# Performance work log

Measured on AMD Instinct MI355X. Metric: run time of the kernel, lower is better.

Reference implementation:

```python
import jax, jax.numpy as jnp
import numpy as np
from jax import lax

B, S, E = 1, 8192, 64
KSZ = 2
THRESHOLD = 0.0
GAMMA = 1.0
OUT_DIM = 4


def setup_inputs() -> dict:
    key = jax.random.key(0)
    ks = jax.random.split(key, 12)
    def lin(k, fan_in, fan_out):
        bound = 1.0 / np.sqrt(fan_in)
        kw, kb = jax.random.split(k)
        W = jax.random.uniform(kw, (fan_in, fan_out), jnp.float32, -bound, bound)
        b = jax.random.uniform(kb, (fan_out,), jnp.float32, -bound, bound)
        return W, b
    x = jax.random.normal(ks[0], (B, S, E), jnp.float32)
    cb = 1.0 / np.sqrt(KSZ * KSZ)
    conv_w = jax.random.uniform(ks[1], (1, 1, KSZ, KSZ), jnp.float32, -cb, cb)
    conv_b = jax.random.uniform(ks[2], (1,), jnp.float32, -cb, cb)
    Wq, bq = lin(ks[3], E, E)
    Wk, bk = lin(ks[4], E, E)
    Wv, bv = lin(ks[5], E, E)
    Wp, bp = lin(ks[6], E, OUT_DIM)
    return {"x": x, "conv_w": conv_w, "conv_b": conv_b, "Wq": Wq, "bq": bq,
            "Wk": Wk, "bk": bk, "Wv": Wv, "bv": bv, "Wp": Wp, "bp": bp}


def reference(x, conv_w, conv_b, Wq, bq, Wk, bk, Wv, bv, Wp, bp):
    # conv pre-filter: (B,S,E) -> (B,1,E,S) -> scalar per batch
    patched = jnp.transpose(x, (0, 2, 1))[:, None]  # (B,1,E,S)
    logits = lax.conv_general_dilated(
        patched, conv_w, (1, 1), "VALID",
        dimension_numbers=("NCHW", "OIHW", "NCHW")) + conv_b[None, :, None, None]
    conv_feat = jax.nn.sigmoid(logits - THRESHOLD).mean(axis=(2, 3))  # (B,1)
    conv_feat = conv_feat.reshape(B)[:, None]  # (B,1)

    # classical scaled dot-product attention (note: no output projection in source)
    scale = E ** (-0.5)
    q = x @ Wq + bq
    k = x @ Wk + bk
    v = x @ Wv + bv
    scores = jnp.einsum("bse,bte->bst", q, k) * scale  # (B,S,S)
    attn = jax.nn.softmax(scores, axis=-1)
    attn_out = jnp.einsum("bst,bte->bse", attn, v)  # (B,S,E)

    # RBF reweighting (identically 1 since x==y, computed faithfully)
    diff = attn_out - attn_out
    kernel_vals = jnp.exp(-GAMMA * jnp.sum(diff * diff, axis=-1, keepdims=True))  # (B,S,1)

    weighted = attn_out * conv_feat * kernel_vals  # broadcast valid since B==1
    pooled = weighted.mean(axis=1)  # (B,E)
    return pooled @ Wp + bp  # (B,4)
```

## Files before the change

### kernel.cpp

```cpp
#include <hip/hip_runtime.h>
#include <hip/hip_bf16.h>

#define S_LEN 8192
#define E_DIM 64
#define NCONV (63 * 8191)
#define PTS 56
#define SVT (S_LEN + 32)

typedef short short8 __attribute__((ext_vector_type(8)));
typedef float f32x4 __attribute__((ext_vector_type(4)));

__device__ __forceinline__ float ldin(const void* __restrict__ p, int i, int f32flag) {
    return f32flag ? ((const float*)p)[i]
                   : __bfloat162float(((const __hip_bfloat16*)p)[i]);
}
__device__ __forceinline__ float bfbits2f(unsigned int u16bits) {
    union { unsigned int u; float f; } c; c.u = u16bits << 16; return c.f;
}
__device__ __forceinline__ unsigned short f2bfu(float f) {
    __hip_bfloat16 h = __float2bfloat16(f);
    union { __hip_bfloat16 h; unsigned short u; } c; c.h = h; return c.u;
}
__device__ __forceinline__ int hw_bad(unsigned short h) {
    const unsigned int e = (h >> 7) & 0xFF;
    return !(h == 0 || h == 0x8000 || (e >= 0x60 && e <= 0x86));
}

__global__ __launch_bounds__(256) void qkv_proj(
    const void* __restrict__ x,
    const void* __restrict__ Wq, const void* __restrict__ bq,
    const void* __restrict__ Wk, const void* __restrict__ bk,
    const void* __restrict__ Wv, const void* __restrict__ bv,
    unsigned short* __restrict__ q_bf, unsigned short* __restrict__ k_bf,
    unsigned short* __restrict__ vT_bf)
{
    __shared__ float wsh[3][4096];
    __shared__ float xT[64 * 16];
    __shared__ float bsh[3][64];
    __shared__ float vs[64 * 17];
    __shared__ int s_fx, s_fw;
    const int tid = threadIdx.x;
    const int row0 = blockIdx.x * 16;

    if (tid == 0) { s_fx = 0; s_fw = 0; }
    __syncthreads();
    if (tid < 64) { if (hw_bad(((const unsigned short*)x)[tid])) atomicOr(&s_fx, 1); }
    else if (tid < 128) { if (hw_bad(((const unsigned short*)Wq)[tid - 64])) atomicOr(&s_fw, 1); }
    __syncthreads();
    const int fx = s_fx, fw = s_fw;

    const void* Ws[3] = { Wq, Wk, Wv };
    const void* Bs[3] = { bq, bk, bv };
#pragma unroll
    for (int w = 0; w < 3; ++w) {
        if (fw) {
            const float4* src = (const float4*)Ws[w];
            for (int i = tid; i < 1024; i += 256) {
                float4 v = src[i];
                float* d = &wsh[w][i * 4];
                d[0] = v.x; d[1] = v.y; d[2] = v.z; d[3] = v.w;
            }
            if (tid < 64) bsh[w][tid] = ((const float*)Bs[w])[tid];
        } else {
            const uint4* src = (const uint4*)Ws[w];
            for (int i = tid; i < 512; i += 256) {
                uint4 v = src[i];
                float* d = &wsh[w][i * 8];
                d[0] = bfbits2f(v.x & 0xffff); d[1] = bfbits2f(v.x >> 16);
                d[2] = bfbits2f(v.y & 0xffff); d[3] = bfbits2f(v.y >> 16);
                d[4] = bfbits2f(v.z & 0xffff); d[5] = bfbits2f(v.z >> 16);
                d[6] = bfbits2f(v.w & 0xffff); d[7] = bfbits2f(v.w >> 16);
            }
            if (tid < 64) bsh[w][tid] = bfbits2f(((const unsigned short*)Bs[w])[tid]);
        }
    }
    for (int idx = tid; idx < 1024; idx += 256) {
        const int r = idx >> 6, i = idx & 63;
        xT[i * 16 + r] = ldin(x, (row0 + r) * 64 + i, fx);
    }
    __syncthreads();

    const int e = tid & 63, rg = tid >> 6;
    float aq[4], ak[4], av[4];
#pragma unroll
    for (int r = 0; r < 4; ++r) { aq[r] = bsh[0][e]; ak[r] = bsh[1][e]; av[r] = bsh[2][e]; }
#pragma unroll 8
    for (int i = 0; i < 64; ++i) {
        const float4 xv = *(const float4*)&xT[i * 16 + rg * 4];
        const float wq = wsh[0][i * 64 + e], wk = wsh[1][i * 64 + e], wv = wsh[2][i * 64 + e];
        aq[0] += xv.x * wq; aq[1] += xv.y * wq; aq[2] += xv.z * wq; aq[3] += xv.w * wq;
        ak[0] += xv.x * wk; ak[1] += xv.y * wk; ak[2] += xv.z * wk; ak[3] += xv.w * wk;
        av[0] += xv.x * wv; av[1] += xv.y * wv; av[2] += xv.z * wv; av[3] += xv.w * wv;
    }
#pragma unroll
    for (int r = 0; r < 4; ++r) {
        const int row = row0 + rg * 4 + r;
        q_bf[row * 64 + e] = f2bfu(aq[r]);
        k_bf[row * 64 + e] = f2bfu(ak[r]);
        vs[e * 17 + rg * 4 + r] = av[r];
    }
    __syncthreads();
    {
        const int e2 = tid >> 2, rp = (tid & 3) * 4;
        const unsigned short h0 = f2bfu(vs[e2 * 17 + rp + 0]);
        const unsigned short h1 = f2bfu(vs[e2 * 17 + rp + 1]);
        const unsigned short h2 = f2bfu(vs[e2 * 17 + rp + 2]);
        const unsigned short h3 = f2bfu(vs[e2 * 17 + rp + 3]);
        uint2 pk;
        pk.x = (unsigned int)h0 | ((unsigned int)h1 << 16);
        pk.y = (unsigned int)h2 | ((unsigned int)h3 << 16);
        *(uint2*)(vT_bf + (size_t)e2 * SVT + row0 + rp) = pk;
    }
}

__global__ __launch_bounds__(256) void conv_reduce(
    const void* __restrict__ x,
    const void* __restrict__ conv_w,
    const void* __restrict__ conv_b,
    const void* __restrict__ Wq,
    float* __restrict__ conv_part)
{
    __shared__ int s_fx, s_fw;
    const int tid = threadIdx.x;
    if (tid == 0) { s_fx = 0; s_fw = 0; }
    __syncthreads();
    if (tid < 64) { if (hw_bad(((const unsigned short*)x)[tid])) atomicOr(&s_fx, 1); }
    else if (tid < 128) { if (hw_bad(((const unsigned short*)Wq)[tid - 64])) atomicOr(&s_fw, 1); }
    __syncthreads();
    const int fx = s_fx, fw = s_fw;

    const float c0 = ldin(conv_w, 0, fw), c1 = ldin(conv_w, 1, fw);
    const float c2 = ldin(conv_w, 2, fw), c3 = ldin(conv_w, 3, fw);
    const float cb = ldin(conv_b, 0, fw);
    float acc = 0.f;
    for (int idx = blockIdx.x * 256 + tid; idx < NCONV; idx += 256 * 256) {
        const int h = idx % 63;
        const int w = idx / 63;
        const float z = c0 * ldin(x, w * 64 + h, fx)     + c1 * ldin(x, (w + 1) * 64 + h, fx)
                      + c2 * ldin(x, w * 64 + h + 1, fx) + c3 * ldin(x, (w + 1) * 64 + h + 1, fx)
                      + cb;
        acc += 1.f / (1.f + __expf(-z));
    }
    for (int off = 32; off > 0; off >>= 1) acc += __shfl_down(acc, off);
    __shared__ float wsum[4];
    if ((tid & 63) == 0) wsum[tid >> 6] = acc;
    __syncthreads();
    if (tid == 0) conv_part[blockIdx.x] = wsum[0] + wsum[1] + wsum[2] + wsum[3];
}

__global__ __launch_bounds__(256, 2) void attn_bf(
    const unsigned short* __restrict__ q_bf, const unsigned short* __restrict__ k_bf,
    const unsigned short* __restrict__ vT_bf,
    unsigned short* __restrict__ o_split, float* __restrict__ l_split, int krange)
{
    __shared__ unsigned short pT[2][4][2][16 * PTS];
    const int tid = threadIdx.x;
    const int wave = tid >> 6, lane = tid & 63;
    const int ln = lane & 15, quad = lane >> 4;
    const int qrow0 = blockIdx.x * 128 + wave * 32;
    const int kbase = blockIdx.y * krange;

    const short8 aQA0 = *(const short8*)(q_bf + (qrow0 + ln) * 64 + quad * 8);
    const short8 aQA1 = *(const short8*)(q_bf + (qrow0 + ln) * 64 + 32 + quad * 8);
    const short8 aQB0 = *(const short8*)(q_bf + (qrow0 + 16 + ln) * 64 + quad * 8);
    const short8 aQB1 = *(const short8*)(q_bf + (qrow0 + 16 + ln) * 64 + 32 + quad * 8);

    const f32x4 zero = {0.f, 0.f, 0.f, 0.f};
    f32x4 oA0 = zero, oA1 = zero, oA2 = zero, oA3 = zero;
    f32x4 oB0 = zero, oB1 = zero, oB2 = zero, oB3 = zero;
    float lA[4] = {0.f, 0.f, 0.f, 0.f}, lB[4] = {0.f, 0.f, 0.f, 0.f};

    const int nIter = krange >> 5;
#pragma unroll 2
    for (int kc = 0; kc < nIter; ++kc) {
        const int key0 = kbase + kc * 32;
        const unsigned short* kb = k_bf + (size_t)key0 * 64;
        const short8 b00 = *(const short8*)(kb + ln * 64 + quad * 8);
        const short8 b01 = *(const short8*)(kb + ln * 64 + 32 + quad * 8);
        const short8 b10 = *(const short8*)(kb + (16 + ln) * 64 + quad * 8);
        const short8 b11 = *(const short8*)(kb + (16 + ln) * 64 + 32 + quad * 8);
        const unsigned short* vb = vT_bf + key0 + quad * 8;
        const short8 v0 = *(const short8*)(vb + (size_t)(0 * 16 + ln) * SVT);
        const short8 v1 = *(const short8*)(vb + (size_t)(1 * 16 + ln) * SVT);
        const short8 v2 = *(const short8*)(vb + (size_t)(2 * 16 + ln) * SVT);
        const short8 v3 = *(const short8*)(vb + (size_t)(3 * 16 + ln) * SVT);

        f32x4 scA0 = __builtin_amdgcn_mfma_f32_16x16x32_bf16(aQA0, b00, zero, 0, 0, 0);
        scA0 = __builtin_amdgcn_mfma_f32_16x16x32_bf16(aQA1, b01, scA0, 0, 0, 0);
        f32x4 scA1 = __builtin_amdgcn_mfma_f32_16x16x32_bf16(aQA0, b10, zero, 0, 0, 0);
        scA1 = __builtin_amdgcn_mfma_f32_16x16x32_bf16(aQA1, b11, scA1, 0, 0, 0);
        f32x4 scB0 = __builtin_amdgcn_mfma_f32_16x16x32_bf16(aQB0, b00, zero, 0, 0, 0);
        scB0 = __builtin_amdgcn_mfma_f32_16x16x32_bf16(aQB1, b01, scB0, 0, 0, 0);
        f32x4 scB1 = __builtin_amdgcn_mfma_f32_16x16x32_bf16(aQB0, b10, zero, 0, 0, 0);
        scB1 = __builtin_amdgcn_mfma_f32_16x16x32_bf16(aQB1, b11, scB1, 0, 0, 0);

        unsigned short* wA = &pT[kc & 1][wave][0][0];
        unsigned short* wB = &pT[kc & 1][wave][1][0];
#pragma unroll
        for (int r = 0; r < 4; ++r) {
            const float pA0 = __expf(scA0[r] * 0.125f);
            const float pA1 = __expf(scA1[r] * 0.125f);
            const float pB0 = __expf(scB0[r] * 0.125f);
            const float pB1 = __expf(scB1[r] * 0.125f);
            lA[r] += pA0 + pA1;
            lB[r] += pB0 + pB1;
            wA[(quad * 4 + r) * PTS + ln]      = f2bfu(pA0);
            wA[(quad * 4 + r) * PTS + 16 + ln] = f2bfu(pA1);
            wB[(quad * 4 + r) * PTS + ln]      = f2bfu(pB0);
            wB[(quad * 4 + r) * PTS + 16 + ln] = f2bfu(pB1);
        }
        const short8 aPA = *(const short8*)(wA + ln * PTS + quad * 8);
        const short8 aPB = *(const short8*)(wB + ln * PTS + quad * 8);

        oA0 = __builtin_amdgcn_mfma_f32_16x16x32_bf16(aPA, v0, oA0, 0, 0, 0);
        oA1 = __builtin_amdgcn_mfma_f32_16x16x32_bf16(aPA, v1, oA1, 0, 0, 0);
        oA2 = __builtin_amdgcn_mfma_f32_16x16x32_bf16(aPA, v2, oA2, 0, 0, 0);
        oA3 = __builtin_amdgcn_mfma_f32_16x16x32_bf16(aPA, v3, oA3, 0, 0, 0);
        oB0 = __builtin_amdgcn_mfma_f32_16x16x32_bf16(aPB, v0, oB0, 0, 0, 0);
        oB1 = __builtin_amdgcn_mfma_f32_16x16x32_bf16(aPB, v1, oB1, 0, 0, 0);
        oB2 = __builtin_amdgcn_mfma_f32_16x16x32_bf16(aPB, v2, oB2, 0, 0, 0);
        oB3 = __builtin_amdgcn_mfma_f32_16x16x32_bf16(aPB, v3, oB3, 0, 0, 0);
    }

    unsigned short* ob = o_split + ((size_t)blockIdx.y * S_LEN + qrow0) * 64;
#pragma unroll
    for (int r = 0; r < 4; ++r) {
        const int rowA = quad * 4 + r;
        ob[rowA * 64 +  0 + ln] = f2bfu(oA0[r]);
        ob[rowA * 64 + 16 + ln] = f2bfu(oA1[r]);
        ob[rowA * 64 + 32 + ln] = f2bfu(oA2[r]);
        ob[rowA * 64 + 48 + ln] = f2bfu(oA3[r]);
        const int rowB = 16 + rowA;
        ob[rowB * 64 +  0 + ln] = f2bfu(oB0[r]);
        ob[rowB * 64 + 16 + ln] = f2bfu(oB1[r]);
        ob[rowB * 64 + 32 + ln] = f2bfu(oB2[r]);
        ob[rowB * 64 + 48 + ln] = f2bfu(oB3[r]);
    }
#pragma unroll
    for (int r = 0; r < 4; ++r) {
        float vA = lA[r], vB = lB[r];
        vA += __shfl_xor(vA, 1); vA += __shfl_xor(vA, 2);
        vA += __shfl_xor(vA, 4); vA += __shfl_xor(vA, 8);
        vB += __shfl_xor(vB, 1); vB += __shfl_xor(vB, 2);
        vB += __shfl_xor(vB, 4); vB += __shfl_xor(vB, 8);
        if (ln == 0) {
            l_split[blockIdx.y * S_LEN + qrow0 + quad * 4 + r]      = vA;
            l_split[blockIdx.y * S_LEN + qrow0 + 16 + quad * 4 + r] = vB;
        }
    }
}

__global__ __launch_bounds__(256) void normalize_pool(
    const unsigned short* __restrict__ o_split, const float* __restrict__ l_split,
    float* __restrict__ pool_part, int ksplit)
{
    __shared__ float psh[64];
    const int tid = threadIdx.x;
    if (tid < 64) psh[tid] = 0.f;
    __syncthreads();
    const int r = blockIdx.x * 32 + (tid >> 3);
    const int c = (tid & 7) * 8;
    float l = 0.f;
    for (int s = 0; s < ksplit; ++s) l += l_split[s * S_LEN + r];
    float o[8] = {0.f, 0.f, 0.f, 0.f, 0.f, 0.f, 0.f, 0.f};
    for (int s = 0; s < ksplit; ++s) {
        const uint4 v = *(const uint4*)(o_split + ((size_t)s * S_LEN + r) * 64 + c);
        o[0] += bfbits2f(v.x & 0xffff); o[1] += bfbits2f(v.x >> 16);
        o[2] += bfbits2f(v.y & 0xffff); o[3] += bfbits2f(v.y >> 16);
        o[4] += bfbits2f(v.z & 0xffff); o[5] += bfbits2f(v.z >> 16);
        o[6] += bfbits2f(v.w & 0xffff); o[7] += bfbits2f(v.w >> 16);
    }
    const float inv = 1.f / l;
#pragma unroll
    for (int j = 0; j < 8; ++j) atomicAdd(&psh[c + j], o[j] * inv);
    __syncthreads();
    if (tid < 64) pool_part[tid * 256 + blockIdx.x] = psh[tid];
}

__global__ void finalize(
    const float* __restrict__ pool_part, const float* __restrict__ conv_part,
    const void* __restrict__ Wp, const void* __restrict__ bp,
    const void* __restrict__ x, const void* __restrict__ Wq,
    void* __restrict__ out)
{
    const int e = threadIdx.x;
    int badx = 0, badw = 0;
    if (hw_bad(((const unsigned short*)x)[e])) badx = 1;
    if (hw_bad(((const unsigned short*)Wq)[e])) badw = 1;
    const int fx = (__ballot(badx) != 0ULL) ? 1 : 0;
    const int fw = (__ballot(badw) != 0ULL) ? 1 : 0;
    const int out_f32 = fx & fw;

    float cv = conv_part[e] + conv_part[64 + e] + conv_part[128 + e] + conv_part[192 + e];
    cv += __shfl_xor(cv, 1); cv += __shfl_xor(cv, 2); cv += __shfl_xor(cv, 4);
    cv += __shfl_xor(cv, 8); cv += __shfl_xor(cv, 16); cv += __shfl_xor(cv, 32);
    const float conv_feat = cv * (1.f / (float)NCONV);
    float pe = 0.f;
    const float4* pp = (const float4*)(pool_part + e * 256);
#pragma unroll 8
    for (int i = 0; i < 64; ++i) {
        const float4 v = pp[i];
        pe += v.x + v.y + v.z + v.w;
    }
    const float pooled = pe * (1.f / (float)S_LEN) * conv_feat;
    float p0 = pooled * ldin(Wp, e * 4 + 0, fw);
    float p1 = pooled * ldin(Wp, e * 4 + 1, fw);
    float p2 = pooled * ldin(Wp, e * 4 + 2, fw);
    float p3 = pooled * ldin(Wp, e * 4 + 3, fw);
    for (int off = 32; off > 0; off >>= 1) {
        p0 += __shfl_down(p0, off);
        p1 += __shfl_down(p1, off);
        p2 += __shfl_down(p2, off);
        p3 += __shfl_down(p3, off);
    }
    if (e == 0) {
        const float r0 = p0 + ldin(bp, 0, fw);
        const float r1 = p1 + ldin(bp, 1, fw);
        const float r2 = p2 + ldin(bp, 2, fw);
        const float r3 = p3 + ldin(bp, 3, fw);
        if (out_f32) {
            float* o = (float*)out;
            o[0] = r0; o[1] = r1; o[2] = r2; o[3] = r3;
        } else {
            __hip_bfloat16* o = (__hip_bfloat16*)out;
            o[0] = __float2bfloat16(r0); o[1] = __float2bfloat16(r1);
            o[2] = __float2bfloat16(r2); o[3] = __float2bfloat16(r3);
        }
    }
}

extern "C" void kernel_launch(void* const* d_in, const int* in_sizes, int n_in,
                              void* d_out, int out_size, void* d_ws, size_t ws_size,
                              hipStream_t stream)
{
    const void* x  = d_in[0];
    const void* cw = d_in[1];
    const void* cb = d_in[2];
    const void* Wq = d_in[3];
    const void* bq = d_in[4];
    const void* Wk = d_in[5];
    const void* bk = d_in[6];
    const void* Wv = d_in[7];
    const void* bv = d_in[8];
    const void* Wp = d_in[9];
    const void* bp = d_in[10];

    auto need = [](int ks) -> size_t {
        return (256 + 64 * 256 + (size_t)ks * S_LEN) * 4
             + (size_t)ks * S_LEN * 64 * 2
             + 2 * (size_t)S_LEN * 64 * 2 + (size_t)64 * SVT * 2 + 1024;
    };
    int ksplit = (ws_size >= need(16)) ? 16 : 8;

    float* ws = (float*)d_ws;
    float* conv_part = ws;
    float* pool_part = ws + 256;
    float* l_split   = ws + 256 + 64 * 256;
    unsigned short* o_split = (unsigned short*)(l_split + (size_t)ksplit * S_LEN);
    unsigned short* q_bf  = o_split + (size_t)ksplit * S_LEN * 64;
    unsigned short* k_bf  = q_bf + (size_t)S_LEN * 64;
    unsigned short* vT_bf = k_bf + (size_t)S_LEN * 64;

    qkv_proj<<<S_LEN / 16, 256, 0, stream>>>(x, Wq, bq, Wk, bk, Wv, bv, q_bf, k_bf, vT_bf);
    conv_reduce<<<256, 256, 0, stream>>>(x, cw, cb, Wq, conv_part);
    attn_bf<<<dim3(S_LEN / 128, ksplit), 256, 0, stream>>>(q_bf, k_bf, vT_bf, o_split, l_split,
                                                            S_LEN / ksplit);
    normalize_pool<<<S_LEN / 32, 256, 0, stream>>>(o_split, l_split, pool_part, ksplit);
    finalize<<<1, 64, 0, stream>>>(pool_part, conv_part, Wp, bp, x, Wq, d_out);
}
```

Baseline: 159.6 us.

## Stage K/V in LDS with double buffering, widen query tile, fuse small kernels

The attention kernel now cooperatively loads each 32-key K/V chunk into double-buffered shared memory, prefetching the next chunk through registers. Each wave now handles 64 query rows instead of 32, so every staged K/V tile feeds more MFMA work. The conv reduction is merged into the QKV projection launch as extra blocks, and normalize and finalize are merged into one kernel that uses global atomics plus a last-block counter. Together these cut global K/V traffic and launch count, at the cost of higher register pressure, half as many attention blocks, and two barriers per key iteration.

After: 177.7 us. 1.11x slower.

```diff
diff --git a/kernel.cpp b/kernel.cpp
--- a/kernel.cpp
+++ b/kernel.cpp
@@ -4,8 +4,10 @@
 #define S_LEN 8192
 #define E_DIM 64
 #define NCONV (63 * 8191)
-#define PTS 56
 #define SVT (S_LEN + 32)
+#define KTS 72
+#define VTS 40
+#define PS  40
 
 typedef short short8 __attribute__((ext_vector_type(8)));
 typedef float f32x4 __attribute__((ext_vector_type(4)));
@@ -26,29 +28,51 @@
     return !(h == 0 || h == 0x8000 || (e >= 0x60 && e <= 0x86));
 }
 
-__global__ __launch_bounds__(256) void qkv_proj(
+__global__ __launch_bounds__(256) void qkv_conv(
     const void* __restrict__ x,
+    const void* __restrict__ conv_w, const void* __restrict__ conv_b,
     const void* __restrict__ Wq, const void* __restrict__ bq,
     const void* __restrict__ Wk, const void* __restrict__ bk,
     const void* __restrict__ Wv, const void* __restrict__ bv,
     unsigned short* __restrict__ q_bf, unsigned short* __restrict__ k_bf,
-    unsigned short* __restrict__ vT_bf)
+    unsigned short* __restrict__ vT_bf, float* __restrict__ conv_part)
 {
+    __shared__ int s_fx, s_fw;
+    const int tid = threadIdx.x;
+    if (tid == 0) { s_fx = 0; s_fw = 0; }
+    __syncthreads();
+    if (tid < 64) { if (hw_bad(((const unsigned short*)x)[tid])) atomicOr(&s_fx, 1); }
+    else if (tid < 128) { if (hw_bad(((const unsigned short*)Wq)[tid - 64])) atomicOr(&s_fw, 1); }
+    __syncthreads();
+    const int fx = s_fx, fw = s_fw;
+
+    if (blockIdx.x >= 512) {
+        const int bid = blockIdx.x - 512;
+        const float c0 = ldin(conv_w, 0, fw), c1 = ldin(conv_w, 1, fw);
+        const float c2 = ldin(conv_w, 2, fw), c3 = ldin(conv_w, 3, fw);
+        const float cb = ldin(conv_b, 0, fw);
+        float acc = 0.f;
+        for (int idx = bid * 256 + tid; idx < NCONV; idx += 64 * 256) {
+            const int h = idx % 63;
+            const int w = idx / 63;
+            const float z = c0 * ldin(x, w * 64 + h, fx)     + c1 * ldin(x, (w + 1) * 64 + h, fx)
+                          + c2 * ldin(x, w * 64 + h + 1, fx) + c3 * ldin(x, (w + 1) * 64 + h + 1, fx)
+                          + cb;
+            acc += 1.f / (1.f + __expf(-z));
+        }
+        for (int off = 32; off > 0; off >>= 1) acc += __shfl_down(acc, off);
+        __shared__ float wsum[4];
+        if ((tid & 63) == 0) wsum[tid >> 6] = acc;
+        __syncthreads();
+        if (tid == 0) conv_part[bid] = wsum[0] + wsum[1] + wsum[2] + wsum[3];
+        return;
+    }
+
     __shared__ float wsh[3][4096];
     __shared__ float xT[64 * 16];
     __shared__ float bsh[3][64];
     __shared__ float vs[64 * 17];
-    __shared__ int s_fx, s_fw;
-    const int tid = threadIdx.x;
     const int row0 = blockIdx.x * 16;
-
-    if (tid == 0) { s_fx = 0; s_fw = 0; }
-    __syncthreads();
-    if (tid < 64) { if (hw_bad(((const unsigned short*)x)[tid])) atomicOr(&s_fx, 1); }
-    else if (tid < 128) { if (hw_bad(((const unsigned short*)Wq)[tid - 64])) atomicOr(&s_fw, 1); }
-    __syncthreads();
-    const int fx = s_fx, fw = s_fw;
-
     const void* Ws[3] = { Wq, Wk, Wv };
     const void* Bs[3] = { bq, bk, bv };
 #pragma unroll
@@ -113,195 +137,174 @@
     }
 }
 
-__global__ __launch_bounds__(256) void conv_reduce(
-    const void* __restrict__ x,
-    const void* __restrict__ conv_w,
-    const void* __restrict__ conv_b,
-    const void* __restrict__ Wq,
-    float* __restrict__ conv_part)
-{
-    __shared__ int s_fx, s_fw;
-    const int tid = threadIdx.x;
-    if (tid == 0) { s_fx = 0; s_fw = 0; }
-    __syncthreads();
-    if (tid < 64) { if (hw_bad(((const unsigned short*)x)[tid])) atomicOr(&s_fx, 1); }
-    else if (tid < 128) { if (hw_bad(((const unsigned short*)Wq)[tid - 64])) atomicOr(&s_fw, 1); }
-    __syncthreads();
-    const int fx = s_fx, fw = s_fw;
-
-    const float c0 = ldin(conv_w, 0, fw), c1 = ldin(conv_w, 1, fw);
-    const float c2 = ldin(conv_w, 2, fw), c3 = ldin(conv_w, 3, fw);
-    const float cb = ldin(conv_b, 0, fw);
-    float acc = 0.f;
-    for (int idx = blockIdx.x * 256 + tid; idx < NCONV; idx += 256 * 256) {
-        const int h = idx % 63;
-        const int w = idx / 63;
-        const float z = c0 * ldin(x, w * 64 + h, fx)     + c1 * ldin(x, (w + 1) * 64 + h, fx)
-                      + c2 * ldin(x, w * 64 + h + 1, fx) + c3 * ldin(x, (w + 1) * 64 + h + 1, fx)
-                      + cb;
-        acc += 1.f / (1.f + __expf(-z));
-    }
-    for (int off = 32; off > 0; off >>= 1) acc += __shfl_down(acc, off);
-    __shared__ float wsum[4];
-    if ((tid & 63) == 0) wsum[tid >> 6] = acc;
-    __syncthreads();
-    if (tid == 0) conv_part[blockIdx.x] = wsum[0] + wsum[1] + wsum[2] + wsum[3];
-}
-
-__global__ __launch_bounds__(256, 2) void attn_bf(
+__global__ __launch_bounds__(256) void attn_bf(
     const unsigned short* __restrict__ q_bf, const unsigned short* __restrict__ k_bf,
     const unsigned short* __restrict__ vT_bf,
     unsigned short* __restrict__ o_split, float* __restrict__ l_split, int krange)
 {
-    __shared__ unsigned short pT[2][4][2][16 * PTS];
+    __shared__ unsigned short kt[2][32 * KTS];
+    __shared__ unsigned short vt[2][64 * VTS];
+    __shared__ unsigned short pTs[4][4][16 * PS];
     const int tid = threadIdx.x;
     const int wave = tid >> 6, lane = tid & 63;
     const int ln = lane & 15, quad = lane >> 4;
-    const int qrow0 = blockIdx.x * 128 + wave * 32;
+    const int qrow0 = blockIdx.x * 256 + wave * 64;
     const int kbase = blockIdx.y * krange;
 
-    const short8 aQA0 = *(const short8*)(q_bf + (qrow0 + ln) * 64 + quad * 8);
-    const short8 aQA1 = *(const short8*)(q_bf + (qrow0 + ln) * 64 + 32 + quad * 8);
-    const short8 aQB0 = *(const short8*)(q_bf + (qrow0 + 16 + ln) * 64 + quad * 8);
-    const short8 aQB1 = *(const short8*)(q_bf + (qrow0 + 16 + ln) * 64 + 32 + quad * 8);
+    short8 aQ[4][2];
+#pragma unroll
+    for (int T = 0; T < 4; ++T) {
+        aQ[T][0] = *(const short8*)(q_bf + (qrow0 + 16 * T + ln) * 64 + quad * 8);
+        aQ[T][1] = *(const short8*)(q_bf + (qrow0 + 16 * T + ln) * 64 + 32 + quad * 8);
+    }
 
     const f32x4 zero = {0.f, 0.f, 0.f, 0.f};
-    f32x4 oA0 = zero, oA1 = zero, oA2 = zero, oA3 = zero;
-    f32x4 oB0 = zero, oB1 = zero, oB2 = zero, oB3 = zero;
-    float lA[4] = {0.f, 0.f, 0.f, 0.f}, lB[4] = {0.f, 0.f, 0.f, 0.f};
+    f32x4 acc[4][4];
+    float l_acc[4][4];
+#pragma unroll
+    for (int T = 0; T < 4; ++T)
+#pragma unroll
+        for (int n = 0; n < 4; ++n) { acc[T][n] = zero; l_acc[T][n] = 0.f; }
+
+    const int krow = tid >> 3, kch = tid & 7;
+    const int vrow = tid >> 2, vch = tid & 3;
+    uint4 kreg, vreg;
+
+    kreg = *(const uint4*)(k_bf + (size_t)(kbase + krow) * 64 + kch * 8);
+    vreg = *(const uint4*)(vT_bf + (size_t)vrow * SVT + kbase + vch * 8);
+    *(uint4*)(&kt[0][krow * KTS + kch * 8]) = kreg;
+    *(uint4*)(&vt[0][vrow * VTS + vch * 8]) = vreg;
+    __syncthreads();
 
     const int nIter = krange >> 5;
 #pragma unroll 2
     for (int kc = 0; kc < nIter; ++kc) {
-        const int key0 = kbase + kc * 32;
-        const unsigned short* kb = k_bf + (size_t)key0 * 64;
-        const short8 b00 = *(const short8*)(kb + ln * 64 + quad * 8);
-        const short8 b01 = *(const short8*)(kb + ln * 64 + 32 + quad * 8);
-        const short8 b10 = *(const short8*)(kb + (16 + ln) * 64 + quad * 8);
-        const short8 b11 = *(const short8*)(kb + (16 + ln) * 64 + 32 + quad * 8);
-        const unsigned short* vb = vT_bf + key0 + quad * 8;
-        const short8 v0 = *(const short8*)(vb + (size_t)(0 * 16 + ln) * SVT);
-        const short8 v1 = *(const short8*)(vb + (size_t)(1 * 16 + ln) * SVT);
-        const short8 v2 = *(const short8*)(vb + (size_t)(2 * 16 + ln) * SVT);
-        const short8 v3 = *(const short8*)(vb + (size_t)(3 * 16 + ln) * SVT);
-
-        f32x4 scA0 = __builtin_amdgcn_mfma_f32_16x16x32_bf16(aQA0, b00, zero, 0, 0, 0);
-        scA0 = __builtin_amdgcn_mfma_f32_16x16x32_bf16(aQA1, b01, scA0, 0, 0, 0);
-        f32x4 scA1 = __builtin_amdgcn_mfma_f32_16x16x32_bf16(aQA0, b10, zero, 0, 0, 0);
-        scA1 = __builtin_amdgcn_mfma_f32_16x16x32_bf16(aQA1, b11, scA1, 0, 0, 0);
-        f32x4 scB0 = __builtin_amdgcn_mfma_f32_16x16x32_bf16(aQB0, b00, zero, 0, 0, 0);
-        scB0 = __builtin_amdgcn_mfma_f32_16x16x32_bf16(aQB1, b01, scB0, 0, 0, 0);
-        f32x4 scB1 = __builtin_amdgcn_mfma_f32_16x16x32_bf16(aQB0, b10, zero, 0, 0, 0);
-        scB1 = __builtin_amdgcn_mfma_f32_16x16x32_bf16(aQB1, b11, scB1, 0, 0, 0);
-
-        unsigned short* wA = &pT[kc & 1][wave][0][0];
-        unsigned short* wB = &pT[kc & 1][wave][1][0];
+        const int cur = kc & 1;
+        if (kc + 1 < nIter) {
+            const int key1 = kbase + (kc + 1) * 32;
+            kreg = *(const uint4*)(k_bf + (size_t)(key1 + krow) * 64 + kch * 8);
+            vreg = *(const uint4*)(vT_bf + (size_t)vrow * SVT + key1 + vch * 8);
+        }
+        const unsigned short* ktc = &kt[cur][0];
+        const unsigned short* vtc = &vt[cur][0];
+        const short8 bE0 = *(const short8*)(ktc + (2 * ln) * KTS + quad * 8);
+        const short8 bE1 = *(const short8*)(ktc + (2 * ln) * KTS + 32 + quad * 8);
+        const short8 bO0 = *(const short8*)(ktc + (2 * ln + 1) * KTS + quad * 8);
+        const short8 bO1 = *(const short8*)(ktc + (2 * ln + 1) * KTS + 32 + quad * 8);
+        const short8 v0 = *(const short8*)(vtc + (0 * 16 + ln) * VTS + quad * 8);
+        const short8 v1 = *(const short8*)(vtc + (1 * 16 + ln) * VTS + quad * 8);
+        const short8 v2 = *(const short8*)(vtc + (2 * 16 + ln) * VTS + quad * 8);
+        const short8 v3 = *(const short8*)(vtc + (3 * 16 + ln) * VTS + quad * 8);
+
+        f32x4 scE[4], scO[4];
+#pragma unroll
+        for (int T = 0; T < 4; ++T) {
+            scE[T] = __builtin_amdgcn_mfma_f32_16x16x32_bf16(aQ[T][0], bE0, zero, 0, 0, 0);
+            scE[T] = __builtin_amdgcn_mfma_f32_16x16x32_bf16(aQ[T][1], bE1, scE[T], 0, 0, 0);
+            scO[T] = __builtin_amdgcn_mfma_f32_16x16x32_bf16(aQ[T][0], bO0, zero, 0, 0, 0);
+            scO[T] = __builtin_amdgcn_mfma_f32_16x16x32_bf16(aQ[T][1], bO1, scO[T], 0, 0, 0);
+        }
+#pragma unroll
+        for (int T = 0; T < 4; ++T) {
+            unsigned short* w = &pTs[wave][T][0];
+#pragma unroll
+            for (int r = 0; r < 4; ++r) {
+                const float pE = __expf(scE[T][r] * 0.125f);
+                const float pO = __expf(scO[T][r] * 0.125f);
+                l_acc[T][r] += pE + pO;
+                const unsigned int pk = (unsigned int)f2bfu(pE) | ((unsigned int)f2bfu(pO) << 16);
+                *(unsigned int*)(w + (quad * 4 + r) * PS + 2 * ln) = pk;
+            }
+        }
+#pragma unroll
+        for (int T = 0; T < 4; ++T) {
+            const short8 aP = *(const short8*)(&pTs[wave][T][ln * PS + quad * 8]);
+            acc[T][0] = __builtin_amdgcn_mfma_f32_16x16x32_bf16(aP, v0, acc[T][0], 0, 0, 0);
+            acc[T][1] = __builtin_amdgcn_mfma_f32_16x16x32_bf16(aP, v1, acc[T][1], 0, 0, 0);
+            acc[T][2] = __builtin_amdgcn_mfma_f32_16x16x32_bf16(aP, v2, acc[T][2], 0, 0, 0);
+            acc[T][3] = __builtin_amdgcn_mfma_f32_16x16x32_bf16(aP, v3, acc[T][3], 0, 0, 0);
+        }
+        __syncthreads();
+        if (kc + 1 < nIter) {
+            *(uint4*)(&kt[cur ^ 1][krow * KTS + kch * 8]) = kreg;
+            *(uint4*)(&vt[cur ^ 1][vrow * VTS + vch * 8]) = vreg;
+        }
+        __syncthreads();
+    }
+
+    unsigned short* ob = o_split + ((size_t)blockIdx.y * S_LEN + qrow0) * 64;
+#pragma unroll
+    for (int T = 0; T < 4; ++T) {
 #pragma unroll
         for (int r = 0; r < 4; ++r) {
-            const float pA0 = __expf(scA0[r] * 0.125f);
-            const float pA1 = __expf(scA1[r] * 0.125f);
-            const float pB0 = __expf(scB0[r] * 0.125f);
-            const float pB1 = __expf(scB1[r] * 0.125f);
-            lA[r] += pA0 + pA1;
-            lB[r] += pB0 + pB1;
-            wA[(quad * 4 + r) * PTS + ln]      = f2bfu(pA0);
-            wA[(quad * 4 + r) * PTS + 16 + ln] = f2bfu(pA1);
-            wB[(quad * 4 + r) * PTS + ln]      = f2bfu(pB0);
-            wB[(quad * 4 + r) * PTS + 16 + ln] = f2bfu(pB1);
-        }
-        const short8 aPA = *(const short8*)(wA + ln * PTS + quad * 8);
-        const short8 aPB = *(const short8*)(wB + ln * PTS + quad * 8);
-
-        oA0 = __builtin_amdgcn_mfma_f32_16x16x32_bf16(aPA, v0, oA0, 0, 0, 0);
-        oA1 = __builtin_amdgcn_mfma_f32_16x16x32_bf16(aPA, v1, oA1, 0, 0, 0);
-        oA2 = __builtin_amdgcn_mfma_f32_16x16x32_bf16(aPA, v2, oA2, 0, 0, 0);
-        oA3 = __builtin_amdgcn_mfma_f32_16x16x32_bf16(aPA, v3, oA3, 0, 0, 0);
-        oB0 = __builtin_amdgcn_mfma_f32_16x16x32_bf16(aPB, v0, oB0, 0, 0, 0);
-        oB1 = __builtin_amdgcn_mfma_f32_16x16x32_bf16(aPB, v1, oB1, 0, 0, 0);
-        oB2 = __builtin_amdgcn_mfma_f32_16x16x32_bf16(aPB, v2, oB2, 0, 0, 0);
-        oB3 = __builtin_amdgcn_mfma_f32_16x16x32_bf16(aPB, v3, oB3, 0, 0, 0);
-    }
-
-    unsigned short* ob = o_split + ((size_t)blockIdx.y * S_LEN + qrow0) * 64;
-#pragma unroll
-    for (int r = 0; r < 4; ++r) {
-        const int rowA = quad * 4 + r;
-        ob[rowA * 64 +  0 + ln] = f2bfu(oA0[r]);
-        ob[rowA * 64 + 16 + ln] = f2bfu(oA1[r]);
-        ob[rowA * 64 + 32 + ln] = f2bfu(oA2[r]);
-        ob[rowA * 64 + 48 + ln] = f2bfu(oA3[r]);
-        const int rowB = 16 + rowA;
-        ob[rowB * 64 +  0 + ln] = f2bfu(oB0[r]);
-        ob[rowB * 64 + 16 + ln] = f2bfu(oB1[r]);
-        ob[rowB * 64 + 32 + ln] = f2bfu(oB2[r]);
-        ob[rowB * 64 + 48 + ln] = f2bfu(oB3[r]);
-    }
-#pragma unroll
-    for (int r = 0; r < 4; ++r) {
-        float vA = lA[r], vB = lB[r];
-        vA += __shfl_xor(vA, 1); vA += __shfl_xor(vA, 2);
-        vA += __shfl_xor(vA, 4); vA += __shfl_xor(vA, 8);
-        vB += __shfl_xor(vB, 1); vB += __shfl_xor(vB, 2);
-        vB += __shfl_xor(vB, 4); vB += __shfl_xor(vB, 8);
-        if (ln == 0) {
-            l_split[blockIdx.y * S_LEN + qrow0 + quad * 4 + r]      = vA;
-            l_split[blockIdx.y * S_LEN + qrow0 + 16 + quad * 4 + r] = vB;
-        }
-    }
-}
-
-__global__ __launch_bounds__(256) void normalize_pool(
+            const int row = 16 * T + quad * 4 + r;
+            ob[row * 64 +  0 + ln] = f2bfu(acc[T][0][r]);
+            ob[row * 64 + 16 + ln] = f2bfu(acc[T][1][r]);
+            ob[row * 64 + 32 + ln] = f2bfu(acc[T][2][r]);
+            ob[row * 64 + 48 + ln] = f2bfu(acc[T][3][r]);
+        }
+#pragma unroll
+        for (int r = 0; r < 4; ++r) {
+            float v = l_acc[T][r];
+            v += __shfl_xor(v, 1); v += __shfl_xor(v, 2);
+            v += __shfl_xor(v, 4); v += __shfl_xor(v, 8);
+            if (ln == 0)
+                l_split[blockIdx.y * S_LEN + qrow0 + 16 * T + quad * 4 + r] = v;
+        }
+    }
+}
+
+__global__ __launch_bounds__(256) void norm_final(
     const unsigned short* __restrict__ o_split, const float* __restrict__ l_split,
-    float* __restrict__ pool_part, int ksplit)
+    float* __restrict__ g_pooled, int* __restrict__ counter,
+    const float* __restrict__ conv_part,
+    const void* __restrict__ Wp, const void* __restrict__ bp,
+    const void* __restrict__ x, const void* __restrict__ Wq,
+    void* __restrict__ out, int ksplit)
 {
     __shared__ float psh[64];
     const int tid = threadIdx.x;
     if (tid < 64) psh[tid] = 0.f;
     __syncthreads();
-    const int r = blockIdx.x * 32 + (tid >> 3);
-    const int c = (tid & 7) * 8;
-    float l = 0.f;
-    for (int s = 0; s < ksplit; ++s) l += l_split[s * S_LEN + r];
-    float o[8] = {0.f, 0.f, 0.f, 0.f, 0.f, 0.f, 0.f, 0.f};
-    for (int s = 0; s < ksplit; ++s) {
-        const uint4 v = *(const uint4*)(o_split + ((size_t)s * S_LEN + r) * 64 + c);
-        o[0] += bfbits2f(v.x & 0xffff); o[1] += bfbits2f(v.x >> 16);
-        o[2] += bfbits2f(v.y & 0xffff); o[3] += bfbits2f(v.y >> 16);
-        o[4] += bfbits2f(v.z & 0xffff); o[5] += bfbits2f(v.z >> 16);
-        o[6] += bfbits2f(v.w & 0xffff); o[7] += bfbits2f(v.w >> 16);
-    }
-    const float inv = 1.f / l;
-#pragma unroll
-    for (int j = 0; j < 8; ++j) atomicAdd(&psh[c + j], o[j] * inv);
-    __syncthreads();
-    if (tid < 64) pool_part[tid * 256 + blockIdx.x] = psh[tid];
-}
-
-__global__ void finalize(
-    const float* __restrict__ pool_part, const float* __restrict__ conv_part,
-    const void* __restrict__ Wp, const void* __restrict__ bp,
-    const void* __restrict__ x, const void* __restrict__ Wq,
-    void* __restrict__ out)
-{
-    const int e = threadIdx.x;
-    int badx = 0, badw = 0;
-    if (hw_bad(((const unsigned short*)x)[e])) badx = 1;
-    if (hw_bad(((const unsigned short*)Wq)[e])) badw = 1;
+#pragma unroll
+    for (int rr = 0; rr < 4; ++rr) {
+        const int r = blockIdx.x * 128 + rr * 32 + (tid >> 3);
+        const int c = (tid & 7) * 8;
+        float l = 0.f;
+        for (int s = 0; s < ksplit; ++s) l += l_split[s * S_LEN + r];
+        float o[8] = {0.f, 0.f, 0.f, 0.f, 0.f, 0.f, 0.f, 0.f};
+        for (int s = 0; s < ksplit; ++s) {
+            const uint4 v = *(const uint4*)(o_split + ((size_t)s * S_LEN + r) * 64 + c);
+            o[0] += bfbits2f(v.x & 0xffff); o[1] += bfbits2f(v.x >> 16);
+            o[2] += bfbits2f(v.y & 0xffff); o[3] += bfbits2f(v.y >> 16);
+            o[4] += bfbits2f(v.z & 0xffff); o[5] += bfbits2f(v.z >> 16);
+            o[6] += bfbits2f(v.w & 0xffff); o[7] += bfbits2f(v.w >> 16);
+        }
+        const float inv = 1.f / l;
+#pragma unroll
+        for (int j = 0; j < 8; ++j) atomicAdd(&psh[c + j], o[j] * inv);
+    }
+    __syncthreads();
+    if (tid < 64) atomicAdd(&g_pooled[tid], psh[tid]);
+    __threadfence();
+    __shared__ int s_last;
+    if (tid == 0) s_last = (atomicAdd(counter, 1) == 63) ? 1 : 0;
+    __syncthreads();
+    if (!s_last || tid >= 64) return;
+
+    __threadfence();
+    const int e = tid;
+    int badx = hw_bad(((const unsigned short*)x)[e]);
+    int badw = hw_bad(((const unsigned short*)Wq)[e]);
     const int fx = (__ballot(badx) != 0ULL) ? 1 : 0;
     const int fw = (__ballot(badw) != 0ULL) ? 1 : 0;
     const int out_f32 = fx & fw;
 
-    float cv = conv_part[e] + conv_part[64 + e] + conv_part[128 + e] + conv_part[192 + e];
+    float cv = conv_part[e];
     cv += __shfl_xor(cv, 1); cv += __shfl_xor(cv, 2); cv += __shfl_xor(cv, 4);
     cv += __shfl_xor(cv, 8); cv += __shfl_xor(cv, 16); cv += __shfl_xor(cv, 32);
     const float conv_feat = cv * (1.f / (float)NCONV);
-    float pe = 0.f;
-    const float4* pp = (const float4*)(pool_part + e * 256);
-#pragma unroll 8
-    for (int i = 0; i < 64; ++i) {
-        const float4 v = pp[i];
-        pe += v.x + v.y + v.z + v.w;
-    }
+    const float pe = atomicAdd(&g_pooled[e], 0.f);
     const float pooled = pe * (1.f / (float)S_LEN) * conv_feat;
     float p0 = pooled * ldin(Wp, e * 4 + 0, fw);
     float p1 = pooled * ldin(Wp, e * 4 + 1, fw);
@@ -346,25 +349,27 @@
     const void* bp = d_in[10];
 
     auto need = [](int ks) -> size_t {
-        return (256 + 64 * 256 + (size_t)ks * S_LEN) * 4
+        return (256 + (size_t)ks * S_LEN) * 4
              + (size_t)ks * S_LEN * 64 * 2
              + 2 * (size_t)S_LEN * 64 * 2 + (size_t)64 * SVT * 2 + 1024;
     };
     int ksplit = (ws_size >= need(16)) ? 16 : 8;
 
     float* ws = (float*)d_ws;
-    float* conv_part = ws;
-    float* pool_part = ws + 256;
-    float* l_split   = ws + 256 + 64 * 256;
+    float* g_pooled  = ws;
+    int*   counter   = (int*)(ws + 64);
+    float* conv_part = ws + 128;
+    float* l_split   = ws + 256;
     unsigned short* o_split = (unsigned short*)(l_split + (size_t)ksplit * S_LEN);
     unsigned short* q_bf  = o_split + (size_t)ksplit * S_LEN * 64;
     unsigned short* k_bf  = q_bf + (size_t)S_LEN * 64;
     unsigned short* vT_bf = k_bf + (size_t)S_LEN * 64;
 
-    qkv_proj<<<S_LEN / 16, 256, 0, stream>>>(x, Wq, bq, Wk, bk, Wv, bv, q_bf, k_bf, vT_bf);
-    conv_reduce<<<256, 256, 0, stream>>>(x, cw, cb, Wq, conv_part);
-    attn_bf<<<dim3(S_LEN / 128, ksplit), 256, 0, stream>>>(q_bf, k_bf, vT_bf, o_split, l_split,
+    hipMemsetAsync(d_ws, 0, 512, stream);
+    qkv_conv<<<576, 256, 0, stream>>>(x, cw, cb, Wq, bq, Wk, bk, Wv, bv,
+                                      q_bf, k_bf, vT_bf, conv_part);
+    attn_bf<<<dim3(S_LEN / 256, ksplit), 256, 0, stream>>>(q_bf, k_bf, vT_bf, o_split, l_split,
                                                             S_LEN / ksplit);
-    normalize_pool<<<S_LEN / 32, 256, 0, stream>>>(o_split, l_split, pool_part, ksplit);
-    finalize<<<1, 64, 0, stream>>>(pool_part, conv_part, Wp, bp, x, Wq, d_out);
-}
+    norm_final<<<64, 256, 0, stream>>>(o_split, l_split, g_pooled, counter, conv_part,
+                                       Wp, bp, x, Wq, d_out, ksplit);
+}
```
